# Kernel optimization log

Measured on AMD Instinct MI355X. Metric: run time of the kernel, lower is better.

Reference implementation:

```python
import jax, jax.numpy as jnp
import numpy as np

B, T, C, H = 4, 2048, 1024, 16
HD = C // H


def setup_inputs() -> dict:
    key = jax.random.key(0)
    k1, k2, k3 = jax.random.split(key, 3)
    x = jax.random.normal(k1, (B, T, C), dtype=jnp.float32)
    w_attn = jax.random.normal(k2, (C, 3 * C), dtype=jnp.float32) * (1.0 / np.sqrt(C))
    b_attn = jnp.zeros((3 * C,), dtype=jnp.float32)
    w_proj = jax.random.normal(k3, (C, C), dtype=jnp.float32) * (1.0 / np.sqrt(C))
    b_proj = jnp.zeros((C,), dtype=jnp.float32)
    return {"x": x, "w_attn": w_attn, "b_attn": b_attn, "w_proj": w_proj, "b_proj": b_proj}


def reference(x, w_attn, b_attn, w_proj, b_proj):
    # QKV projection: [B,T,3C]
    qkv = x @ w_attn + b_attn
    q, k, v = jnp.split(qkv, 3, axis=-1)
    # [B,H,T,HD]
    q = q.reshape(B, T, H, HD).swapaxes(1, 2)
    k = k.reshape(B, T, H, HD).swapaxes(1, 2)
    v = v.reshape(B, T, H, HD).swapaxes(1, 2)
    scale = 1.0 / jnp.sqrt(jnp.float32(HD))
    attn = jnp.einsum('bhqd,bhkd->bhqk', q, k) * scale  # [B,H,T,T]
    causal = jnp.tril(jnp.ones((T, T), dtype=bool))
    attn = jnp.where(causal[None, None, :, :], attn, -jnp.inf)
    attn = jax.nn.softmax(attn, axis=-1)
    y = jnp.einsum('bhqk,bhkd->bhqd', attn, v)  # [B,H,T,HD]
    y = y.swapaxes(1, 2).reshape(B, T, C)
    return y @ w_proj + b_proj
```

## Files before the change

kernel.cpp:

```cpp
#include <hip/hip_runtime.h>
#include <hip/hip_bf16.h>

#define BB 4
#define TT 2048
#define CC 1024
#define HH 16
#define HD 64
#define NQ (3*CC)
#define QSCALE 0.18033688011112042f

typedef __attribute__((ext_vector_type(8))) short bf16x8;
typedef __attribute__((ext_vector_type(4))) short short4_t;
typedef __attribute__((ext_vector_type(4))) float f32x4;

#define MFMA(a,b,c) __builtin_amdgcn_mfma_f32_16x16x32_bf16(a,b,c,0,0,0)

#define ASYNC16(gsrc, ldst) \
  __builtin_amdgcn_global_load_lds((const __attribute__((address_space(1))) void*)(gsrc), \
                                   (__attribute__((address_space(3))) void*)(ldst), 16, 0, 0)

#define SWZA(row) (((((row) & 7) + (((row) >> 3) & 3)) & 7) << 3)

static __device__ __forceinline__ short f2bf(float f){
    union { float f; unsigned u; } v; v.f = f;
    unsigned r = v.u + 0x7FFFu + ((v.u >> 16) & 1u);
    return (short)(r >> 16);
}
static __device__ __forceinline__ unsigned cvtpk(float a, float b){
    unsigned r;
    asm("v_cvt_pk_bf16_f32 %0, %1, %2" : "=v"(r) : "v"(a), "v"(b));
    return r;
}

__global__ __launch_bounds__(256)
void convert_x(const float* __restrict__ x, short* __restrict__ xb)
{
    int i = (blockIdx.x * 256 + threadIdx.x) * 8;
    float4 a = *reinterpret_cast<const float4*>(&x[i]);
    float4 b = *reinterpret_cast<const float4*>(&x[i+4]);
    bf16x8 o = { f2bf(a.x), f2bf(a.y), f2bf(a.z), f2bf(a.w),
                 f2bf(b.x), f2bf(b.y), f2bf(b.z), f2bf(b.w) };
    *reinterpret_cast<bf16x8*>(&xb[i]) = o;
}

__global__ __launch_bounds__(256)
void transpose_w(const float* __restrict__ w, short* __restrict__ wT, int N)
{
    __shared__ short sm[64*72];
    const int kt0 = blockIdx.x * 64;
    const int nt0 = blockIdx.y * 64;
    const int t = threadIdx.x;
    const int r  = t >> 4;
    const int c4 = (t & 15) * 4;
#pragma unroll
    for (int it = 0; it < 4; it++){
        int k = r + it*16;
        float4 v = *reinterpret_cast<const float4*>(&w[(size_t)(kt0 + k)*N + nt0 + c4]);
        sm[(c4+0)*72 + k] = f2bf(v.x);
        sm[(c4+1)*72 + k] = f2bf(v.y);
        sm[(c4+2)*72 + k] = f2bf(v.z);
        sm[(c4+3)*72 + k] = f2bf(v.w);
    }
    __syncthreads();
    const int nl = t >> 2;
    const int kc = (t & 3) * 16;
    bf16x8 o0 = *reinterpret_cast<const bf16x8*>(&sm[nl*72 + kc]);
    bf16x8 o1 = *reinterpret_cast<const bf16x8*>(&sm[nl*72 + kc + 8]);
    short* dst = &wT[(size_t)(nt0 + nl)*CC + kt0 + kc];
    *reinterpret_cast<bf16x8*>(dst)     = o0;
    *reinterpret_cast<bf16x8*>(dst + 8) = o1;
}

__global__ __launch_bounds__(256, 2)
void qkv_gemm(const short* __restrict__ xb, const short* __restrict__ wT,
              const float* __restrict__ bias,
              short* __restrict__ qb, short* __restrict__ kb, short* __restrict__ vtb)
{
    __shared__ short smem[128*136];
    short* As = smem;
    short* Bs = smem + 8192;
    const int bid = blockIdx.x;
    const int swz = (bid & 7) * 192 + (bid >> 3);
    const int bm = swz / (NQ/128);
    const int bn = swz % (NQ/128);
    const int m0 = bm*128, n0 = bn*128;
    const int t  = threadIdx.x;
    const int wid = t >> 6, lane = t & 63;
    const int wr = wid >> 1, wc = wid & 1;
    const int l15 = lane & 15, lh = lane >> 4;

    f32x4 acc[4][4];
#pragma unroll
    for (int i=0;i<4;i++)
#pragma unroll
      for (int j=0;j<4;j++) acc[i][j] = (f32x4)0.f;

    for (int k0 = 0; k0 < CC; k0 += 64) {
        __syncthreads();
#pragma unroll
        for (int i=0;i<4;i++){
            int u   = (wid*4 + i)*64 + lane;
            int row = u >> 3, c = u & 7;
            int cs  = c ^ (row & 7);
            ASYNC16(&xb[(size_t)(m0+row)*CC + k0 + cs*8], &As[(wid*4+i)*512]);
            ASYNC16(&wT[(size_t)(n0+row)*CC + k0 + cs*8], &Bs[(wid*4+i)*512]);
        }
        __syncthreads();
#pragma unroll
        for (int ks=0;ks<2;ks++){
            bf16x8 a[4], b[4];
#pragma unroll
            for (int m=0;m<4;m++){
                int row = wr*64 + m*16 + l15;
                a[m] = *reinterpret_cast<const bf16x8*>(&As[row*64 + (((ks<<2)|lh) ^ (row&7))*8]);
            }
#pragma unroll
            for (int n=0;n<4;n++){
                int col = wc*64 + n*16 + l15;
                b[n] = *reinterpret_cast<const bf16x8*>(&Bs[col*64 + (((ks<<2)|lh) ^ (col&7))*8]);
            }
#pragma unroll
            for (int m=0;m<4;m++)
#pragma unroll
              for (int n=0;n<4;n++)
                acc[m][n] = MFMA(a[m], b[n], acc[m][n]);
        }
    }

    if (n0 < 2*CC) {
#pragma unroll
        for (int n=0;n<4;n++){
            int col = n0 + wc*64 + n*16 + l15;
            int sect = col >> 10;
            int cc = col & 1023;
            int h = cc >> 6, d = cc & 63;
            float bv = bias[col];
            short* dst = (sect==0) ? qb : kb;
            float mul = (sect==0) ? QSCALE : 1.f;
#pragma unroll
            for (int m=0;m<4;m++)
#pragma unroll
              for (int r=0;r<4;r++){
                int row = m0 + wr*64 + m*16 + lh*4 + r;
                int b_ = row >> 11, tt_ = row & (TT-1);
                float v = (acc[m][n][r] + bv) * mul;
                dst[((size_t)(b_*HH + h)*TT + tt_)*HD + d] = f2bf(v);
              }
        }
    } else {
        __syncthreads();
        short* Ts = smem;
#pragma unroll
        for (int n=0;n<4;n++){
            int colL = wc*64 + n*16 + l15;
            float bv = bias[n0 + colL];
#pragma unroll
            for (int m=0;m<4;m++){
                int rowL = wr*64 + m*16 + lh*4;
                short4_t pk = { f2bf(acc[m][n][0]+bv), f2bf(acc[m][n][1]+bv),
                                f2bf(acc[m][n][2]+bv), f2bf(acc[m][n][3]+bv) };
                *reinterpret_cast<short4_t*>(&Ts[colL*136 + rowL]) = pk;
            }
        }
        __syncthreads();
        const int b_ = m0 >> 11, t0 = m0 & (TT-1);
        const int cc0 = n0 - 2*CC;
#pragma unroll
        for (int pass=0;pass<2;pass++){
            int c = (t >> 2) + pass*64;
            int vcol = cc0 + c;
            short* dst = vtb + ((size_t)(b_*HH + (vcol>>6))*HD + (vcol&63))*TT + t0;
#pragma unroll
            for (int it=0;it<4;it++){
                int r0 = (t & 3)*8 + it*32;
                *reinterpret_cast<bf16x8*>(&dst[r0]) =
                    *reinterpret_cast<const bf16x8*>(&Ts[c*136 + r0]);
            }
        }
    }
}

__global__ __launch_bounds__(256, 3)
void attn_kernel(const short* __restrict__ qb, const short* __restrict__ kb,
                 const short* __restrict__ vtb, short* __restrict__ yb)
{
    __shared__ short Ks[2][64*64];
    __shared__ short Vt[2][64*64];
    __shared__ short Ps[4][16*64];

    const int bh = blockIdx.x;
    const int qt = 15 - blockIdx.y;
    const int b_ = bh >> 4, h = bh & 15;
    const short* qp  = qb  + (size_t)bh*TT*HD;
    const short* kp  = kb  + (size_t)bh*TT*HD;
    const short* vtp = vtb + (size_t)bh*HD*TT;
    const int t = threadIdx.x, wid = t >> 6, lane = t & 63;
    const int l15 = lane & 15, lh = lane >> 4;

    int kvoffB[8];
#pragma unroll
    for (int ks=0;ks<2;ks++)
#pragma unroll
      for (int i=0;i<4;i++){
        int row = i*16 + l15;
        kvoffB[ks*4+i] = ((row*64 + ks*32 + lh*8) ^ SWZA(row)) * 2;
      }
    int pwB[4];
#pragma unroll
    for (int f=0;f<4;f++)
        pwB[f] = ((l15*64 + f*16 + lh*4) ^ SWZA(l15)) * 2;
    char* KsB = (char*)&Ks[0][0];
    char* VtB = (char*)&Vt[0][0];
    char* PsB = (char*)&Ps[wid][0];

    const int su0 = (wid*2+0)*64 + lane;
    const int su1 = (wid*2+1)*64 + lane;
    const int sr0 = su0 >> 3, sc0 = (su0 & 7) ^ (SWZA(su0 >> 3) >> 3);
    const int sr1 = su1 >> 3, sc1 = (su1 & 7) ^ (SWZA(su1 >> 3) >> 3);

    const short* kg0 = kp  + (size_t)sr0*HD + sc0*8;
    const short* kg1 = kp  + (size_t)sr1*HD + sc1*8;
    const short* vg0 = vtp + (size_t)sr0*TT + sc0*8;
    const short* vg1 = vtp + (size_t)sr1*TT + sc1*8;

    const bf16x8 ones = { 0x3F80,0x3F80,0x3F80,0x3F80,0x3F80,0x3F80,0x3F80,0x3F80 };

    auto stageN = [&](int buf){
        ASYNC16(kg0, &Ks[buf][(wid*2+0)*512]);
        ASYNC16(kg1, &Ks[buf][(wid*2+1)*512]);
        ASYNC16(vg0, &Vt[buf][(wid*2+0)*512]);
        ASYNC16(vg1, &Vt[buf][(wid*2+1)*512]);
        kg0 += 64*HD; kg1 += 64*HD; vg0 += 64; vg1 += 64;
    };

    const int wq0 = qt*128 + wid*32;

    bf16x8 qf[2][2];
#pragma unroll
    for (int m=0;m<2;m++)
#pragma unroll
      for (int ks=0;ks<2;ks++)
        qf[m][ks] = *reinterpret_cast<const bf16x8*>(
            &qp[(size_t)(wq0 + m*16 + l15)*HD + ks*32 + lh*8]);

    f32x4 po[2][4];
    f32x4 pden[2];
#pragma unroll
    for (int m=0;m<2;m++){
        pden[m] = (f32x4)0.f;
#pragma unroll
        for (int n=0;n<4;n++) po[m][n] = (f32x4)0.f;
    }

    const int ntk = 2*(qt + 1);

    stageN(0);
    __syncthreads();

    for (int kt = 0; kt < ntk; ){
#pragma unroll
        for (int cur = 0; cur < 2; cur++, kt++){
            const int kv0 = kt*64;
            if (kt+1 < ntk) stageN(cur ^ 1);

            if (kv0 <= wq0 + 31){
                f32x4 s[2][4];
#pragma unroll
                for (int m=0;m<2;m++)
#pragma unroll
                  for (int f=0;f<4;f++) s[m][f] = (f32x4)0.f;
                __builtin_amdgcn_s_setprio(1);
#pragma unroll
                for (int ks=0;ks<2;ks++){
#pragma unroll
                    for (int f=0;f<4;f++){
                        bf16x8 kf = *reinterpret_cast<const bf16x8*>(
                            KsB + cur*8192 + kvoffB[ks*4+f]);
                        s[0][f] = MFMA(kf, qf[0][ks], s[0][f]);
                        s[1][f] = MFMA(kf, qf[1][ks], s[1][f]);
                    }
                }
                __builtin_amdgcn_s_setprio(0);
#pragma unroll
                for (int m=0;m<2;m++){
                    if (kv0 + 63 > wq0 + m*16){
                        int qm = wq0 + m*16 + l15;
#pragma unroll
                        for (int f=0;f<4;f++)
#pragma unroll
                          for (int r=0;r<4;r++){
                            int kv = kv0 + f*16 + lh*4 + r;
                            if (kv > qm) s[m][f][r] = -1e30f;
                          }
                    }
                }
#pragma unroll
                for (int m=0;m<2;m++){
#pragma unroll
                    for (int f=0;f<4;f++){
                        uint2 pk;
                        pk.x = cvtpk(exp2f(s[m][f][0]), exp2f(s[m][f][1]));
                        pk.y = cvtpk(exp2f(s[m][f][2]), exp2f(s[m][f][3]));
                        *reinterpret_cast<uint2*>(PsB + pwB[f]) = pk;
                    }
                    __builtin_amdgcn_s_setprio(1);
#pragma unroll
                    for (int k2=0;k2<2;k2++){
                        bf16x8 pa = *reinterpret_cast<const bf16x8*>(PsB + kvoffB[k2*4]);
                        pden[m] = MFMA(pa, ones, pden[m]);
#pragma unroll
                        for (int n=0;n<4;n++){
                            bf16x8 vf = *reinterpret_cast<const bf16x8*>(
                                VtB + cur*8192 + kvoffB[k2*4+n]);
                            po[m][n] = MFMA(pa, vf, po[m][n]);
                        }
                    }
                    __builtin_amdgcn_s_setprio(0);
                }
            }

            __syncthreads();
        }
    }

#pragma unroll
    for (int m=0;m<2;m++){
        float rcp[4];
#pragma unroll
        for (int r=0;r<4;r++) rcp[r] = 1.f / pden[m][r];
#pragma unroll
        for (int n=0;n<4;n++)
#pragma unroll
          for (int r=0;r<4;r++){
            int q = wq0 + m*16 + lh*4 + r;
            int dd = n*16 + l15;
            yb[(size_t)(b_*TT + q)*CC + h*HD + dd] = f2bf(po[m][n][r] * rcp[r]);
          }
    }
}

__global__ __launch_bounds__(256, 2)
void proj_gemm(const short* __restrict__ y, const short* __restrict__ wpT,
               const float* __restrict__ bias, float* __restrict__ out)
{
    __shared__ short As[128*64];
    __shared__ short Bs[128*64];
    const int bid = blockIdx.x;
    const int swz = (bid & 7) * 64 + (bid >> 3);
    const int bm = swz >> 3, bn = swz & 7;
    const int m0 = bm*128, n0 = bn*128;
    const int t  = threadIdx.x;
    const int wid = t >> 6, lane = t & 63;
    const int wr = wid >> 1, wc = wid & 1;
    const int l15 = lane & 15, lh = lane >> 4;

    f32x4 acc[4][4];
#pragma unroll
    for (int i=0;i<4;i++)
#pragma unroll
      for (int j=0;j<4;j++) acc[i][j] = (f32x4)0.f;

    for (int k0 = 0; k0 < CC; k0 += 64) {
        __syncthreads();
#pragma unroll
        for (int i=0;i<4;i++){
            int u   = (wid*4 + i)*64 + lane;
            int row = u >> 3, c = u & 7;
            int cs  = c ^ (row & 7);
            ASYNC16(&y[(size_t)(m0+row)*CC + k0 + cs*8],   &As[(wid*4+i)*512]);
            ASYNC16(&wpT[(size_t)(n0+row)*CC + k0 + cs*8], &Bs[(wid*4+i)*512]);
        }
        __syncthreads();
#pragma unroll
        for (int ks=0;ks<2;ks++){
            bf16x8 a[4], b[4];
#pragma unroll
            for (int m=0;m<4;m++){
                int row = wr*64 + m*16 + l15;
                a[m] = *reinterpret_cast<const bf16x8*>(&As[row*64 + (((ks<<2)|lh) ^ (row&7))*8]);
            }
#pragma unroll
            for (int n=0;n<4;n++){
                int col = wc*64 + n*16 + l15;
                b[n] = *reinterpret_cast<const bf16x8*>(&Bs[col*64 + (((ks<<2)|lh) ^ (col&7))*8]);
            }
#pragma unroll
            for (int m=0;m<4;m++)
#pragma unroll
              for (int n=0;n<4;n++)
                acc[m][n] = MFMA(a[m], b[n], acc[m][n]);
        }
    }

#pragma unroll
    for (int n=0;n<4;n++){
        int col = n0 + wc*64 + n*16 + l15;
        float bv = bias[col];
#pragma unroll
        for (int m=0;m<4;m++)
#pragma unroll
          for (int r=0;r<4;r++){
            int row = m0 + wr*64 + m*16 + lh*4 + r;
            out[(size_t)row*CC + col] = acc[m][n][r] + bv;
          }
    }
}

extern "C" void kernel_launch(void* const* d_in, const int* in_sizes, int n_in,
                              void* d_out, int out_size, void* d_ws, size_t ws_size,
                              hipStream_t stream) {
    const float* x      = (const float*)d_in[0];
    const float* w_attn = (const float*)d_in[1];
    const float* b_attn = (const float*)d_in[2];
    const float* w_proj = (const float*)d_in[3];
    const float* b_proj = (const float*)d_in[4];
    float* out = (float*)d_out;

    const size_t S = (size_t)BB*TT*CC;
    short* qb  = (short*)d_ws;
    short* kb  = qb + S;
    short* vtb = kb + S;
    short* yx  = vtb + S;
    short* wT  = yx + S;
    short* wpT = wT + (size_t)NQ*CC;

    convert_x<<<dim3(S/(256*8)), 256, 0, stream>>>(x, yx);
    transpose_w<<<dim3(CC/64, NQ/64), 256, 0, stream>>>(w_attn, wT, NQ);
    transpose_w<<<dim3(CC/64, CC/64), 256, 0, stream>>>(w_proj, wpT, CC);
    qkv_gemm<<<dim3((BB*TT/128)*(NQ/128)), 256, 0, stream>>>(yx, wT, b_attn, qb, kb, vtb);
    attn_kernel<<<dim3(BB*HH, TT/128), 256, 0, stream>>>(qb, kb, vtb, yx);
    proj_gemm<<<dim3((BB*TT/128)*(CC/128)), 256, 0, stream>>>(yx, wpT, b_proj, out);
}
```

Baseline: 171.2 us.

## Load K/V fragments directly from global into registers per wave, dropping LDS staging

Result: slower. 244.2 us (+42.7%).

```diff
diff --git a/kernel.cpp b/kernel.cpp
--- a/kernel.cpp
+++ b/kernel.cpp
@@ -180,12 +180,10 @@
     }
 }
 
-__global__ __launch_bounds__(256, 3)
+__global__ __launch_bounds__(256, 2)
 void attn_kernel(const short* __restrict__ qb, const short* __restrict__ kb,
                  const short* __restrict__ vtb, short* __restrict__ yb)
 {
-    __shared__ short Ks[2][64*64];
-    __shared__ short Vt[2][64*64];
     __shared__ short Ps[4][16*64];
 
     const int bh = blockIdx.x;
@@ -197,41 +195,15 @@
     const int t = threadIdx.x, wid = t >> 6, lane = t & 63;
     const int l15 = lane & 15, lh = lane >> 4;
 
-    int kvoffB[8];
-#pragma unroll
-    for (int ks=0;ks<2;ks++)
-#pragma unroll
-      for (int i=0;i<4;i++){
-        int row = i*16 + l15;
-        kvoffB[ks*4+i] = ((row*64 + ks*32 + lh*8) ^ SWZA(row)) * 2;
-      }
     int pwB[4];
 #pragma unroll
     for (int f=0;f<4;f++)
         pwB[f] = ((l15*64 + f*16 + lh*4) ^ SWZA(l15)) * 2;
-    char* KsB = (char*)&Ks[0][0];
-    char* VtB = (char*)&Vt[0][0];
+    int prB[2];
+#pragma unroll
+    for (int ks=0;ks<2;ks++)
+        prB[ks] = ((l15*64 + ks*32 + lh*8) ^ SWZA(l15)) * 2;
     char* PsB = (char*)&Ps[wid][0];
-
-    const int su0 = (wid*2+0)*64 + lane;
-    const int su1 = (wid*2+1)*64 + lane;
-    const int sr0 = su0 >> 3, sc0 = (su0 & 7) ^ (SWZA(su0 >> 3) >> 3);
-    const int sr1 = su1 >> 3, sc1 = (su1 & 7) ^ (SWZA(su1 >> 3) >> 3);
-
-    const short* kg0 = kp  + (size_t)sr0*HD + sc0*8;
-    const short* kg1 = kp  + (size_t)sr1*HD + sc1*8;
-    const short* vg0 = vtp + (size_t)sr0*TT + sc0*8;
-    const short* vg1 = vtp + (size_t)sr1*TT + sc1*8;
-
-    const bf16x8 ones = { 0x3F80,0x3F80,0x3F80,0x3F80,0x3F80,0x3F80,0x3F80,0x3F80 };
-
-    auto stageN = [&](int buf){
-        ASYNC16(kg0, &Ks[buf][(wid*2+0)*512]);
-        ASYNC16(kg1, &Ks[buf][(wid*2+1)*512]);
-        ASYNC16(vg0, &Vt[buf][(wid*2+0)*512]);
-        ASYNC16(vg1, &Vt[buf][(wid*2+1)*512]);
-        kg0 += 64*HD; kg1 += 64*HD; vg0 += 64; vg1 += 64;
-    };
 
     const int wq0 = qt*128 + wid*32;
 
@@ -243,6 +215,9 @@
         qf[m][ks] = *reinterpret_cast<const bf16x8*>(
             &qp[(size_t)(wq0 + m*16 + l15)*HD + ks*32 + lh*8]);
 
+    const short* kfp = kp  + (size_t)l15*HD + lh*8;
+    const short* vfp = vtp + (size_t)l15*TT + lh*8;
+
     f32x4 po[2][4];
     f32x4 pden[2];
 #pragma unroll
@@ -252,74 +227,93 @@
         for (int n=0;n<4;n++) po[m][n] = (f32x4)0.f;
     }
 
-    const int ntk = 2*(qt + 1);
-
-    stageN(0);
-    __syncthreads();
-
-    for (int kt = 0; kt < ntk; ){
-#pragma unroll
-        for (int cur = 0; cur < 2; cur++, kt++){
-            const int kv0 = kt*64;
-            if (kt+1 < ntk) stageN(cur ^ 1);
-
-            if (kv0 <= wq0 + 31){
-                f32x4 s[2][4];
-#pragma unroll
-                for (int m=0;m<2;m++)
-#pragma unroll
-                  for (int f=0;f<4;f++) s[m][f] = (f32x4)0.f;
-                __builtin_amdgcn_s_setprio(1);
-#pragma unroll
-                for (int ks=0;ks<2;ks++){
-#pragma unroll
-                    for (int f=0;f<4;f++){
-                        bf16x8 kf = *reinterpret_cast<const bf16x8*>(
-                            KsB + cur*8192 + kvoffB[ks*4+f]);
-                        s[0][f] = MFMA(kf, qf[0][ks], s[0][f]);
-                        s[1][f] = MFMA(kf, qf[1][ks], s[1][f]);
-                    }
-                }
-                __builtin_amdgcn_s_setprio(0);
-#pragma unroll
-                for (int m=0;m<2;m++){
-                    if (kv0 + 63 > wq0 + m*16){
-                        int qm = wq0 + m*16 + l15;
-#pragma unroll
-                        for (int f=0;f<4;f++)
-#pragma unroll
-                          for (int r=0;r<4;r++){
-                            int kv = kv0 + f*16 + lh*4 + r;
-                            if (kv > qm) s[m][f][r] = -1e30f;
-                          }
-                    }
-                }
-#pragma unroll
-                for (int m=0;m<2;m++){
-#pragma unroll
-                    for (int f=0;f<4;f++){
-                        uint2 pk;
-                        pk.x = cvtpk(exp2f(s[m][f][0]), exp2f(s[m][f][1]));
-                        pk.y = cvtpk(exp2f(s[m][f][2]), exp2f(s[m][f][3]));
-                        *reinterpret_cast<uint2*>(PsB + pwB[f]) = pk;
-                    }
-                    __builtin_amdgcn_s_setprio(1);
-#pragma unroll
-                    for (int k2=0;k2<2;k2++){
-                        bf16x8 pa = *reinterpret_cast<const bf16x8*>(PsB + kvoffB[k2*4]);
-                        pden[m] = MFMA(pa, ones, pden[m]);
-#pragma unroll
-                        for (int n=0;n<4;n++){
-                            bf16x8 vf = *reinterpret_cast<const bf16x8*>(
-                                VtB + cur*8192 + kvoffB[k2*4+n]);
-                            po[m][n] = MFMA(pa, vf, po[m][n]);
-                        }
-                    }
-                    __builtin_amdgcn_s_setprio(0);
-                }
-            }
-
-            __syncthreads();
+    const bf16x8 ones = { 0x3F80,0x3F80,0x3F80,0x3F80,0x3F80,0x3F80,0x3F80,0x3F80 };
+
+    const int ntkw = ((wq0 + 31) >> 6) + 1;
+
+    bf16x8 kf[2][4], vf[2][4];
+#pragma unroll
+    for (int ks=0;ks<2;ks++)
+#pragma unroll
+      for (int f=0;f<4;f++)
+        kf[ks][f] = *reinterpret_cast<const bf16x8*>(kfp + (size_t)(f*16)*HD + ks*32);
+#pragma unroll
+    for (int ks=0;ks<2;ks++)
+#pragma unroll
+      for (int n=0;n<4;n++)
+        vf[ks][n] = *reinterpret_cast<const bf16x8*>(vfp + (size_t)(n*16)*TT + ks*32);
+
+    for (int kt = 0; kt < ntkw; kt++){
+        const int kv0 = kt*64;
+        const bool pf = (kt+1 < ntkw);
+
+        f32x4 s[2][4];
+#pragma unroll
+        for (int m=0;m<2;m++)
+#pragma unroll
+          for (int f=0;f<4;f++) s[m][f] = (f32x4)0.f;
+        __builtin_amdgcn_s_setprio(1);
+#pragma unroll
+        for (int ks=0;ks<2;ks++){
+#pragma unroll
+            for (int f=0;f<4;f++){
+                s[0][f] = MFMA(kf[ks][f], qf[0][ks], s[0][f]);
+                s[1][f] = MFMA(kf[ks][f], qf[1][ks], s[1][f]);
+            }
+        }
+        __builtin_amdgcn_s_setprio(0);
+
+        if (pf){
+#pragma unroll
+            for (int ks=0;ks<2;ks++)
+#pragma unroll
+              for (int f=0;f<4;f++)
+                kf[ks][f] = *reinterpret_cast<const bf16x8*>(
+                    kfp + (size_t)(kv0 + 64 + f*16)*HD + ks*32);
+        }
+
+#pragma unroll
+        for (int m=0;m<2;m++){
+            if (kv0 + 63 > wq0 + m*16){
+                int qm = wq0 + m*16 + l15;
+#pragma unroll
+                for (int f=0;f<4;f++)
+#pragma unroll
+                  for (int r=0;r<4;r++){
+                    int kv = kv0 + f*16 + lh*4 + r;
+                    if (kv > qm) s[m][f][r] = -1e30f;
+                  }
+            }
+        }
+
+#pragma unroll
+        for (int m=0;m<2;m++){
+#pragma unroll
+            for (int f=0;f<4;f++){
+                uint2 pk;
+                pk.x = cvtpk(exp2f(s[m][f][0]), exp2f(s[m][f][1]));
+                pk.y = cvtpk(exp2f(s[m][f][2]), exp2f(s[m][f][3]));
+                *reinterpret_cast<uint2*>(PsB + pwB[f]) = pk;
+            }
+            __builtin_amdgcn_s_setprio(1);
+#pragma unroll
+            for (int k2=0;k2<2;k2++){
+                bf16x8 pa = *reinterpret_cast<const bf16x8*>(PsB + prB[k2]);
+                pden[m] = MFMA(pa, ones, pden[m]);
+#pragma unroll
+                for (int n=0;n<4;n++)
+                    po[m][n] = MFMA(pa, vf[k2][n], po[m][n]);
+            }
+            __builtin_amdgcn_s_setprio(0);
+        }
+
+        if (pf){
+#pragma unroll
+            for (int ks=0;ks<2;ks++)
+#pragma unroll
+              for (int n=0;n<4;n++)
+                vf[ks][n] = *reinterpret_cast<const bf16x8*>(
+                    vfp + (size_t)(n*16)*TT + kv0 + 64 + ks*32);
         }
     }
 
```
